# Kernel optimization log

Hardware: AMD Instinct MI355X
Metric: run time of the kernel (lower is better)

Reference implementation:

```python
import jax, jax.numpy as jnp
import numpy as np

B, T, C, H = 4, 2048, 1024, 16
D = C // H  # head_size = 64


def setup_inputs() -> dict:
    key = jax.random.key(0)
    k1, k2, k3 = jax.random.split(key, 3)
    h = jax.random.normal(k1, (B, T, C), dtype=jnp.float32)
    # additive float mask, [B,1,1,T]; zeros = no padding
    attention_mask = jnp.zeros((B, 1, 1, T), dtype=jnp.float32)
    # learned params (bias=False linears), scaled like default torch init
    w_attn = jax.random.normal(k2, (C, 3 * C), dtype=jnp.float32) / np.sqrt(C)
    w_proj = jax.random.normal(k3, (C, C), dtype=jnp.float32) / np.sqrt(C)
    return {"h": h, "attention_mask": attention_mask, "w_attn": w_attn, "w_proj": w_proj}


def reference(h, attention_mask, w_attn, w_proj):
    # fused QKV projection: [B,T,3C]
    qkv = jnp.einsum("btc,cd->btd", h, w_attn)
    q, k, v = jnp.split(qkv, 3, axis=-1)
    # [B,T,C] -> [B,H,T,D]
    def to_heads(x):
        return x.reshape(B, T, H, D).transpose(0, 2, 1, 3)
    q, k, v = to_heads(q), to_heads(k), to_heads(v)
    # scaled dot-product attention with additive mask (non-causal)
    scale = 1.0 / np.sqrt(D).astype(np.float32)
    scores = jnp.einsum("bhqd,bhkd->bhqk", q, k) * scale + attention_mask
    probs = jax.nn.softmax(scores, axis=-1)
    y = jnp.einsum("bhqk,bhkd->bhqd", probs, v)
    # [B,H,T,D] -> [B,T,C]
    y = y.transpose(0, 2, 1, 3).reshape(B, T, C)
    return jnp.einsum("btc,cd->btd", y, w_proj)
```

## Files before the change

### kernel.cpp

```cpp
#include <hip/hip_runtime.h>
#include <hip/hip_bf16.h>

#define DEV static __device__ __forceinline__

typedef __attribute__((ext_vector_type(4))) float f32x4;
typedef __attribute__((ext_vector_type(8))) short bf16x8;

constexpr int Bb = 4, Ts = 2048, Cc = 1024, Hh = 16, Dd = 64;
constexpr int Mm = Bb * Ts;
constexpr float SCQ = 0.18033688f;

union frag_u {
  bf16x8 f;
  uint2  u2[2];
  ushort us[8];
  uint4  u4;
};

DEV ushort f2bf(float x) {
  union { float f; unsigned u; } v; v.f = x;
  unsigned r = v.u + 0x7FFFu + ((v.u >> 16) & 1u);
  return (ushort)(r >> 16);
}

DEV ushort f2bf_hw(float x) {
  union { __hip_bfloat16 b; ushort u; } cv;
  cv.b = __float2bfloat16(x);
  return cv.u;
}

typedef const __attribute__((address_space(1))) unsigned int gu32;
typedef __attribute__((address_space(3))) unsigned int lu32;
DEV void gload16(const void* g, void* l) {
  __builtin_amdgcn_global_load_lds((gu32*)g, (lu32*)l, 16, 0, 0);
}

DEV void ld_frag16(frag_u& fr, const ushort* lds, int row, int chunk) {
  int off = row * 128 + ((chunk ^ (row & 7)) << 4);
  fr.u4 = *reinterpret_cast<const uint4*>(reinterpret_cast<const char*>(lds) + off);
}
DEV void lds_st64p(ushort* lds, int row, int p, uint2 v) {
  int off = row * 128 + ((((p >> 3) ^ (row & 7)) << 4) | ((2 * p) & 15));
  *reinterpret_cast<uint2*>(reinterpret_cast<char*>(lds) + off) = v;
}

__global__ __launch_bounds__(256) void cvt_kernel(const float* __restrict__ in,
                                                  ushort* __restrict__ out, int n4) {
  for (int i = blockIdx.x * blockDim.x + threadIdx.x; i < n4;
       i += gridDim.x * blockDim.x) {
    float4 v = reinterpret_cast<const float4*>(in)[i];
    ushort4 o;
    o.x = f2bf(v.x); o.y = f2bf(v.y); o.z = f2bf(v.z); o.w = f2bf(v.w);
    reinterpret_cast<ushort4*>(out)[i] = o;
  }
}

__global__ __launch_bounds__(256) void expmask_kernel(const float* __restrict__ m,
                                                      float* __restrict__ em, int n) {
  int i = blockIdx.x * blockDim.x + threadIdx.x;
  if (i < n) em[i] = __expf(m[i]);
}

__global__ __launch_bounds__(256) void transpose_cvt(const float* __restrict__ in,
                                                     ushort* __restrict__ out,
                                                     int R, int Ccols) {
  __shared__ float tile[32][33];
  int c0 = blockIdx.x * 32, r0 = blockIdx.y * 32;
  int tx = threadIdx.x & 31, ty = threadIdx.x >> 5;
#pragma unroll
  for (int i = 0; i < 4; ++i) {
    int r = ty + i * 8;
    tile[r][tx] = in[(size_t)(r0 + r) * Ccols + c0 + tx];
  }
  __syncthreads();
#pragma unroll
  for (int i = 0; i < 4; ++i) {
    int r = ty + i * 8;
    out[(size_t)(c0 + r) * R + r0 + tx] = f2bf(tile[tx][r]);
  }
}

template <int EPI>
__global__ __launch_bounds__(256) void gemm_bt(const ushort* __restrict__ A,
                                               const ushort* __restrict__ Bt,
                                               int M, int N, int K,
                                               float* __restrict__ Cf,
                                               ushort* __restrict__ Qb,
                                               ushort* __restrict__ Kb,
                                               ushort* __restrict__ Vb,
                                               const float* __restrict__ expm) {
  __shared__ ushort Al[2][128 * 64];
  __shared__ ushort Bl[2][128 * 64];
  const int tid = threadIdx.x;
  const int lane = tid & 63, wid = tid >> 6;
  const int g = lane >> 4, l15 = lane & 15;
  const int wr = wid >> 1, wc = wid & 1;
  const int m0 = blockIdx.y * 128, n0 = blockIdx.x * 128;

#define ISSUE(slot, kt)                                                         \
  {                                                                             \
    _Pragma("unroll") for (int it = 0; it < 4; ++it) {                          \
      int chunk = wid * 256 + it * 64 + lane;                                   \
      int row = chunk >> 3, c16 = (chunk & 7) ^ (row & 7);                      \
      gload16(A + (size_t)(m0 + row) * K + (kt) * 64 + c16 * 8,                 \
              Al[slot] + (size_t)(wid * 256 + it * 64) * 8);                    \
      gload16(Bt + (size_t)(n0 + row) * K + (kt) * 64 + c16 * 8,                \
              Bl[slot] + (size_t)(wid * 256 + it * 64) * 8);                    \
    }                                                                           \
  }

  f32x4 acc[4][4];
#pragma unroll
  for (int i = 0; i < 4; ++i)
#pragma unroll
    for (int j = 0; j < 4; ++j) acc[i][j] = f32x4{0.f, 0.f, 0.f, 0.f};

  const int nkt = K >> 6;
  ISSUE(0, 0);
  __syncthreads();
  for (int kt = 0; kt < nkt; ++kt) {
    const int s = kt & 1;
    if (kt + 1 < nkt) ISSUE(s ^ 1, kt + 1);
#pragma unroll
    for (int ks = 0; ks < 2; ++ks) {
      frag_u af[4], bfr[4];
#pragma unroll
      for (int i = 0; i < 4; ++i) {
        ld_frag16(af[i], Al[s], wr * 64 + i * 16 + l15, 4 * ks + g);
        ld_frag16(bfr[i], Bl[s], wc * 64 + i * 16 + l15, 4 * ks + g);
      }
#pragma unroll
      for (int i = 0; i < 4; ++i)
#pragma unroll
        for (int j = 0; j < 4; ++j)
          acc[i][j] = __builtin_amdgcn_mfma_f32_16x16x32_bf16(af[i].f, bfr[j].f,
                                                              acc[i][j], 0, 0, 0);
    }
    __syncthreads();
  }
#undef ISSUE

#pragma unroll
  for (int i = 0; i < 4; ++i)
#pragma unroll
    for (int j = 0; j < 4; ++j) {
      int mrow = m0 + wr * 64 + i * 16 + 4 * g;
      int ncol = n0 + wc * 64 + j * 16 + l15;
#pragma unroll
      for (int r = 0; r < 4; ++r) {
        float v = acc[i][j][r];
        int m = mrow + r;
        if (EPI == 0) {
          Cf[(size_t)m * N + ncol] = v;
        } else {
          int which = ncol >> 10, c = ncol & 1023;
          int hd = c >> 6, d = c & 63;
          int b = m >> 11, t = m & 2047;
          size_t idx;
          if (which == 2) {
            v *= expm[(size_t)b * Ts + t];
            idx = (((size_t)(b * Hh + hd)) * Dd + d) * Ts + t;
          } else {
            if (which == 0) v *= SCQ;
            idx = (((size_t)(b * Hh + hd)) * Ts + t) * Dd + d;
          }
          ushort bv = f2bf(v);
          ushort* dst = (which == 0) ? Qb : (which == 1) ? Kb : Vb;
          dst[idx] = bv;
        }
      }
    }
}

__global__ __launch_bounds__(512, 4) void attn_kernel(const ushort* __restrict__ Qb,
                                                      const ushort* __restrict__ Kb,
                                                      const ushort* __restrict__ VTb,
                                                      const float* __restrict__ expm,
                                                      ushort* __restrict__ Yb) {
  __shared__ ushort Klds[2][64 * 64];
  __shared__ ushort Vlds[2][64 * 64];
  __shared__ ushort wlds[2][64];

  const int tid = threadIdx.x;
  const int lane = tid & 63, wid = tid >> 6;
  const int g = lane >> 4, l15 = lane & 15;
  const int bh = blockIdx.x;
  const int b = bh >> 4, h = bh & 15;
  const int qt = blockIdx.y;

  const ushort* Qh = Qb + (size_t)bh * Ts * Dd;
  const ushort* Kh = Kb + (size_t)bh * Ts * Dd;
  const ushort* Vh = VTb + (size_t)bh * Dd * Ts;
  const float* erow = expm + (size_t)b * Ts;

  const int krow = tid >> 3, kpos = tid & 7;
  const int kc16 = kpos ^ (krow & 7);
  const int srow = tid >> 3, sc16 = tid & 7;
  const int vp0 = 32 * (sc16 >> 2) + 16 * (sc16 & 1) + 4 * ((sc16 >> 1) & 1);
  const int wp = (tid & 32) | ((tid & 12) << 1) | ((tid & 16) >> 2) | (tid & 3);

  frag_u aq[2][2];
#pragma unroll
  for (int qsub = 0; qsub < 2; ++qsub) {
    const ushort* qp = Qh + (size_t)(qt * 256 + wid * 32 + qsub * 16 + l15) * Dd;
#pragma unroll
    for (int ks = 0; ks < 2; ++ks)
      aq[qsub][ks].u4 = *reinterpret_cast<const uint4*>(qp + ks * 32 + 8 * g);
  }

  f32x4 acc[2][4];
  f32x4 lacc[2];
#pragma unroll
  for (int q = 0; q < 2; ++q) {
    lacc[q] = f32x4{0.f, 0.f, 0.f, 0.f};
#pragma unroll
    for (int dt = 0; dt < 4; ++dt) acc[q][dt] = f32x4{0.f, 0.f, 0.f, 0.f};
  }

  uint4 vreg;
  float wreg = 0.f;

#define ISSUE(kt, buf)                                                          \
  gload16(Kh + (size_t)((kt) * 64 + krow) * Dd + kc16 * 8,                      \
          Klds[buf] + (size_t)(wid * 64) * 8);                                  \
  vreg = *reinterpret_cast<const uint4*>(Vh + (size_t)srow * Ts + (kt) * 64 + sc16 * 8); \
  wreg = (tid < 64) ? erow[(kt) * 64 + tid] : 0.f;

#define COMMIT(buf)                                                             \
  lds_st64p(Vlds[buf], srow, vp0, uint2{vreg.x, vreg.y});                       \
  lds_st64p(Vlds[buf], srow, vp0 + 8, uint2{vreg.z, vreg.w});                   \
  if (tid < 64) wlds[buf][wp] = f2bf_hw(wreg);

  ISSUE(0, 0);
  COMMIT(0);
  __syncthreads();

  const int NT = Ts / 64;
  for (int kt = 0; kt < NT; ++kt) {
    const int cur = kt & 1;
    const bool more = (kt + 1 < NT);
    if (more) { ISSUE(kt + 1, cur ^ 1); }

    f32x4 s[2][4];
#pragma unroll
    for (int q = 0; q < 2; ++q)
#pragma unroll
      for (int n = 0; n < 4; ++n) s[q][n] = f32x4{0.f, 0.f, 0.f, 0.f};
    __builtin_amdgcn_s_setprio(1);
#pragma unroll
    for (int ks = 0; ks < 2; ++ks)
#pragma unroll
      for (int n = 0; n < 4; ++n) {
        frag_u bk;
        ld_frag16(bk, Klds[cur], n * 16 + l15, 4 * ks + g);
#pragma unroll
        for (int q = 0; q < 2; ++q)
          s[q][n] = __builtin_amdgcn_mfma_f32_16x16x32_bf16(bk.f, aq[q][ks].f,
                                                            s[q][n], 0, 0, 0);
      }
    __builtin_amdgcn_s_setprio(0);

    frag_u pa[2][2];
#pragma unroll
    for (int q = 0; q < 2; ++q)
#pragma unroll
      for (int n = 0; n < 4; ++n)
#pragma unroll
        for (int r = 0; r < 4; ++r)
          pa[q][n >> 1].us[(n & 1) * 4 + r] =
              f2bf_hw(__builtin_amdgcn_exp2f(s[q][n][r]));

    frag_u wf[2];
    wf[0].u4 = *reinterpret_cast<const uint4*>(&wlds[cur][8 * g]);
    wf[1].u4 = *reinterpret_cast<const uint4*>(&wlds[cur][32 + 8 * g]);
    __builtin_amdgcn_s_setprio(1);
#pragma unroll
    for (int ks = 0; ks < 2; ++ks)
#pragma unroll
      for (int q = 0; q < 2; ++q)
        lacc[q] = __builtin_amdgcn_mfma_f32_16x16x32_bf16(pa[q][ks].f, wf[ks].f,
                                                          lacc[q], 0, 0, 0);
#pragma unroll
    for (int ks = 0; ks < 2; ++ks)
#pragma unroll
      for (int dt = 0; dt < 4; ++dt) {
        frag_u bv;
        ld_frag16(bv, Vlds[cur], dt * 16 + l15, 4 * ks + g);
#pragma unroll
        for (int q = 0; q < 2; ++q)
          acc[q][dt] = __builtin_amdgcn_mfma_f32_16x16x32_bf16(pa[q][ks].f, bv.f,
                                                               acc[q][dt], 0, 0, 0);
      }
    __builtin_amdgcn_s_setprio(0);

    if (more) { COMMIT(cur ^ 1); }
    __syncthreads();
  }
#undef ISSUE
#undef COMMIT

#pragma unroll
  for (int q = 0; q < 2; ++q) {
#pragma unroll
    for (int r = 0; r < 4; ++r) {
      float inv = 1.0f / lacc[q][r];
      int t = qt * 256 + wid * 32 + q * 16 + 4 * g + r;
      size_t base = ((size_t)(b * Ts + t)) * Cc + h * Dd;
#pragma unroll
      for (int dt = 0; dt < 4; ++dt)
        Yb[base + dt * 16 + l15] = f2bf(acc[q][dt][r] * inv);
    }
  }
}

extern "C" void kernel_launch(void* const* d_in, const int* in_sizes, int n_in,
                              void* d_out, int out_size, void* d_ws, size_t ws_size,
                              hipStream_t stream) {
  const float* h    = (const float*)d_in[0];
  const float* mask = (const float*)d_in[1];
  const float* wa   = (const float*)d_in[2];
  const float* wp   = (const float*)d_in[3];
  float* out = (float*)d_out;

  char* ws = (char*)d_ws;
  ushort* hbf     = (ushort*)(ws);
  ushort* wattn_t = (ushort*)(ws + (16u << 20));
  ushort* wproj_t = (ushort*)(ws + (22u << 20));
  ushort* Qb      = (ushort*)(ws + (24u << 20));
  ushort* Kb      = (ushort*)(ws + (40u << 20));
  ushort* VTb     = (ushort*)(ws + (56u << 20));
  float*  expm    = (float*)(ws + (72u << 20));
  ushort* Ybf = hbf;

  cvt_kernel<<<2048, 256, 0, stream>>>(h, hbf, (Mm * Cc) / 4);
  expmask_kernel<<<(Bb * Ts + 255) / 256, 256, 0, stream>>>(mask, expm, Bb * Ts);
  transpose_cvt<<<dim3(3 * Cc / 32, Cc / 32), 256, 0, stream>>>(wa, wattn_t, Cc, 3 * Cc);
  transpose_cvt<<<dim3(Cc / 32, Cc / 32), 256, 0, stream>>>(wp, wproj_t, Cc, Cc);

  gemm_bt<1><<<dim3(3 * Cc / 128, Mm / 128), 256, 0, stream>>>(
      hbf, wattn_t, Mm, 3 * Cc, Cc, nullptr, Qb, Kb, VTb, expm);

  attn_kernel<<<dim3(Bb * Hh, Ts / 256), 512, 0, stream>>>(Qb, Kb, VTb, expm, Ybf);

  gemm_bt<0><<<dim3(Cc / 128, Mm / 128), 256, 0, stream>>>(
      Ybf, wproj_t, Mm, Cc, Cc, out, nullptr, nullptr, nullptr, nullptr);
}
```

Baseline: 203.4 us.

## Load GEMM B operand directly to registers and stage QKV epilogue through LDS

The GEMM no longer stages the B (weight) tile in LDS. Each wave loads its B fragments straight from global memory into double-buffered registers, and the k-loop is unrolled by two so register and LDS buffers alternate. The QKV epilogue now writes scaled bf16 results into a swizzled LDS tile and then emits coalesced 16-byte global stores for Q/K and the transposed V, replacing scattered 2-byte stores. The mask exponentials are cached once per block in shared memory. In exchange, register pressure rises and the B fragment loads from global memory are uncoalesced per-lane 16-byte reads.

```diff
diff --git a/kernel.cpp b/kernel.cpp
--- a/kernel.cpp
+++ b/kernel.cpp
@@ -42,6 +42,19 @@
 DEV void lds_st64p(ushort* lds, int row, int p, uint2 v) {
   int off = row * 128 + ((((p >> 3) ^ (row & 7)) << 4) | ((2 * p) & 15));
   *reinterpret_cast<uint2*>(reinterpret_cast<char*>(lds) + off) = v;
+}
+
+DEV void eW16(char* E, int row, int col, ushort v) {
+  int off = row * 256 + ((((col >> 3) ^ (row & 7)) << 4) | ((col & 7) * 2));
+  *reinterpret_cast<ushort*>(E + off) = v;
+}
+DEV void eW64(char* E, int row, int col, uint2 v) {
+  int off = row * 256 + ((((col >> 3) ^ (row & 7)) << 4) | ((col & 7) * 2));
+  *reinterpret_cast<uint2*>(E + off) = v;
+}
+DEV uint4 eR128(const char* E, int row, int dc) {
+  int off = row * 256 + ((dc ^ (row & 7)) << 4);
+  return *reinterpret_cast<const uint4*>(E + off);
 }
 
 __global__ __launch_bounds__(256) void cvt_kernel(const float* __restrict__ in,
@@ -90,86 +103,137 @@
                                                ushort* __restrict__ Vb,
                                                const float* __restrict__ expm) {
   __shared__ ushort Al[2][128 * 64];
-  __shared__ ushort Bl[2][128 * 64];
+  __shared__ float evals[128];
   const int tid = threadIdx.x;
   const int lane = tid & 63, wid = tid >> 6;
   const int g = lane >> 4, l15 = lane & 15;
   const int wr = wid >> 1, wc = wid & 1;
   const int m0 = blockIdx.y * 128, n0 = blockIdx.x * 128;
 
-#define ISSUE(slot, kt)                                                         \
+  if (EPI == 1 && tid < 128)
+    evals[tid] = expm[(size_t)(m0 >> 11) * Ts + (m0 & 2047) + tid];
+
+#define AISSUE(slot, t)                                                         \
   {                                                                             \
     _Pragma("unroll") for (int it = 0; it < 4; ++it) {                          \
       int chunk = wid * 256 + it * 64 + lane;                                   \
       int row = chunk >> 3, c16 = (chunk & 7) ^ (row & 7);                      \
-      gload16(A + (size_t)(m0 + row) * K + (kt) * 64 + c16 * 8,                 \
+      gload16(A + (size_t)(m0 + row) * K + (t) * 64 + c16 * 8,                  \
               Al[slot] + (size_t)(wid * 256 + it * 64) * 8);                    \
-      gload16(Bt + (size_t)(n0 + row) * K + (kt) * 64 + c16 * 8,                \
-              Bl[slot] + (size_t)(wid * 256 + it * 64) * 8);                    \
     }                                                                           \
   }
 
+#define BLOAD(breg, t)                                                          \
+  _Pragma("unroll") for (int j = 0; j < 4; ++j)                                 \
+    _Pragma("unroll") for (int ks = 0; ks < 2; ++ks)                            \
+      breg[j][ks].u4 = *reinterpret_cast<const uint4*>(                         \
+          Bt + (size_t)(n0 + wc * 64 + j * 16 + l15) * K + (t) * 64 + ks * 32 + 8 * g);
+
+#define COMPUTE(s, breg)                                                        \
+  _Pragma("unroll") for (int ks = 0; ks < 2; ++ks) {                            \
+    frag_u af[4];                                                               \
+    _Pragma("unroll") for (int i = 0; i < 4; ++i)                               \
+      ld_frag16(af[i], Al[s], wr * 64 + i * 16 + l15, 4 * ks + g);              \
+    _Pragma("unroll") for (int i = 0; i < 4; ++i)                               \
+      _Pragma("unroll") for (int j = 0; j < 4; ++j)                             \
+        acc[i][j] = __builtin_amdgcn_mfma_f32_16x16x32_bf16(af[i].f,            \
+                        breg[j][ks].f, acc[i][j], 0, 0, 0);                     \
+  }
+
   f32x4 acc[4][4];
 #pragma unroll
   for (int i = 0; i < 4; ++i)
 #pragma unroll
     for (int j = 0; j < 4; ++j) acc[i][j] = f32x4{0.f, 0.f, 0.f, 0.f};
 
+  frag_u b0[4][2], b1[4][2];
   const int nkt = K >> 6;
-  ISSUE(0, 0);
+
+  BLOAD(b0, 0);
+  AISSUE(0, 0);
   __syncthreads();
-  for (int kt = 0; kt < nkt; ++kt) {
-    const int s = kt & 1;
-    if (kt + 1 < nkt) ISSUE(s ^ 1, kt + 1);
-#pragma unroll
-    for (int ks = 0; ks < 2; ++ks) {
-      frag_u af[4], bfr[4];
+  for (int kt = 0; kt < nkt; kt += 2) {
+    BLOAD(b1, kt + 1);
+    AISSUE(1, kt + 1);
+    COMPUTE(0, b0);
+    __syncthreads();
+    if (kt + 2 < nkt) { BLOAD(b0, kt + 2); AISSUE(0, kt + 2); }
+    COMPUTE(1, b1);
+    __syncthreads();
+  }
+#undef AISSUE
+#undef BLOAD
+#undef COMPUTE
+
+  if (EPI == 0) {
+#pragma unroll
+    for (int i = 0; i < 4; ++i)
+#pragma unroll
+      for (int j = 0; j < 4; ++j) {
+        int mrow = m0 + wr * 64 + i * 16 + 4 * g;
+        int ncol = n0 + wc * 64 + j * 16 + l15;
+#pragma unroll
+        for (int r = 0; r < 4; ++r)
+          Cf[(size_t)(mrow + r) * N + ncol] = acc[i][j][r];
+      }
+  } else {
+    char* E = reinterpret_cast<char*>(&Al[0][0]);
+    const int seg = n0 >> 10;
+    const int hd0 = (n0 & 1023) >> 6;
+    const int bq = m0 >> 11, tt0 = m0 & 2047;
+    if (seg < 2) {
+      const float vs = (seg == 0) ? SCQ : 1.0f;
+#pragma unroll
+      for (int i = 0; i < 4; ++i)
+#pragma unroll
+        for (int j = 0; j < 4; ++j) {
+          int tb = wr * 64 + i * 16 + 4 * g;
+          int ncol = wc * 64 + j * 16 + l15;
+#pragma unroll
+          for (int r = 0; r < 4; ++r)
+            eW16(E, tb + r, ncol, f2bf(acc[i][j][r] * vs));
+        }
+      __syncthreads();
+      ushort* dstQ = (seg == 0) ? Qb : Kb;
+#pragma unroll
+      for (int h2 = 0; h2 < 2; ++h2) {
+        ushort* gb = dstQ + ((size_t)(bq * Hh + hd0 + h2) * Ts + tt0) * Dd;
+#pragma unroll
+        for (int k = 0; k < 4; ++k) {
+          int c = k * 256 + tid;
+          int tt = c >> 3, d16 = c & 7;
+          uint4 v = eR128(E, tt, h2 * 8 + d16);
+          *reinterpret_cast<uint4*>(gb + (size_t)c * 8) = v;
+        }
+      }
+    } else {
 #pragma unroll
       for (int i = 0; i < 4; ++i) {
-        ld_frag16(af[i], Al[s], wr * 64 + i * 16 + l15, 4 * ks + g);
-        ld_frag16(bfr[i], Bl[s], wc * 64 + i * 16 + l15, 4 * ks + g);
-      }
-#pragma unroll
-      for (int i = 0; i < 4; ++i)
-#pragma unroll
-        for (int j = 0; j < 4; ++j)
-          acc[i][j] = __builtin_amdgcn_mfma_f32_16x16x32_bf16(af[i].f, bfr[j].f,
-                                                              acc[i][j], 0, 0, 0);
+        int tb = wr * 64 + i * 16 + 4 * g;
+        float e0 = evals[tb], e1 = evals[tb + 1];
+        float e2 = evals[tb + 2], e3 = evals[tb + 3];
+#pragma unroll
+        for (int j = 0; j < 4; ++j) {
+          int ncol = wc * 64 + j * 16 + l15;
+          unsigned lo = (unsigned)f2bf(acc[i][j][0] * e0) |
+                        ((unsigned)f2bf(acc[i][j][1] * e1) << 16);
+          unsigned hi = (unsigned)f2bf(acc[i][j][2] * e2) |
+                        ((unsigned)f2bf(acc[i][j][3] * e3) << 16);
+          eW64(E, ncol, tb, uint2{lo, hi});
+        }
+      }
+      __syncthreads();
+#pragma unroll
+      for (int k = 0; k < 8; ++k) {
+        int c = k * 256 + tid;
+        int row = c >> 4, t16 = c & 15;
+        int hd = hd0 + (row >> 6), d = row & 63;
+        uint4 v = eR128(E, row, t16);
+        ushort* gb = Vb + ((size_t)(bq * Hh + hd) * Dd + d) * Ts + tt0;
+        *reinterpret_cast<uint4*>(gb + (size_t)t16 * 8) = v;
+      }
     }
-    __syncthreads();
-  }
-#undef ISSUE
-
-#pragma unroll
-  for (int i = 0; i < 4; ++i)
-#pragma unroll
-    for (int j = 0; j < 4; ++j) {
-      int mrow = m0 + wr * 64 + i * 16 + 4 * g;
-      int ncol = n0 + wc * 64 + j * 16 + l15;
-#pragma unroll
-      for (int r = 0; r < 4; ++r) {
-        float v = acc[i][j][r];
-        int m = mrow + r;
-        if (EPI == 0) {
-          Cf[(size_t)m * N + ncol] = v;
-        } else {
-          int which = ncol >> 10, c = ncol & 1023;
-          int hd = c >> 6, d = c & 63;
-          int b = m >> 11, t = m & 2047;
-          size_t idx;
-          if (which == 2) {
-            v *= expm[(size_t)b * Ts + t];
-            idx = (((size_t)(b * Hh + hd)) * Dd + d) * Ts + t;
-          } else {
-            if (which == 0) v *= SCQ;
-            idx = (((size_t)(b * Hh + hd)) * Ts + t) * Dd + d;
-          }
-          ushort bv = f2bf(v);
-          ushort* dst = (which == 0) ? Qb : (which == 1) ? Kb : Vb;
-          dst[idx] = bv;
-        }
-      }
-    }
+  }
 }
 
 __global__ __launch_bounds__(512, 4) void attn_kernel(const ushort* __restrict__ Qb,
```

Measured after the change: 251.6 us. 23.7% more time.

## Switch GEMM to 32x32 MFMA, single-buffer LDS, staged V-transpose epilogue

Applied to the files above, without the earlier changes.

The GEMM moves from 16x16x32 to 32x32x16 bf16 MFMA tiles and drops the double-buffered LDS prefetch for a single buffer with load-then-sync. This halves LDS use, which may raise occupancy, but global-to-LDS loads no longer overlap with compute. The QKV epilogue is specialised per block segment, hoisting branch decisions and caching the mask exponentials in shared memory. The transposed V output is staged through a swizzled LDS tile so it can be written with coalesced 16-byte stores instead of scattered 2-byte writes.

```diff
diff --git a/kernel.cpp b/kernel.cpp
--- a/kernel.cpp
+++ b/kernel.cpp
@@ -4,6 +4,7 @@
 #define DEV static __device__ __forceinline__
 
 typedef __attribute__((ext_vector_type(4))) float f32x4;
+typedef __attribute__((ext_vector_type(16))) float f32x16;
 typedef __attribute__((ext_vector_type(8))) short bf16x8;
 
 constexpr int Bb = 4, Ts = 2048, Cc = 1024, Hh = 16, Dd = 64;
@@ -42,6 +43,15 @@
 DEV void lds_st64p(ushort* lds, int row, int p, uint2 v) {
   int off = row * 128 + ((((p >> 3) ^ (row & 7)) << 4) | ((2 * p) & 15));
   *reinterpret_cast<uint2*>(reinterpret_cast<char*>(lds) + off) = v;
+}
+
+DEV void eW64b(char* E, int row, int col, uint2 v) {
+  int off = row * 256 + ((((col >> 3) ^ (row & 15)) << 4) | ((col & 7) * 2));
+  *reinterpret_cast<uint2*>(E + off) = v;
+}
+DEV uint4 eR128b(const char* E, int row, int dc) {
+  int off = row * 256 + ((dc ^ (row & 15)) << 4);
+  return *reinterpret_cast<const uint4*>(E + off);
 }
 
 __global__ __launch_bounds__(256) void cvt_kernel(const float* __restrict__ in,
@@ -89,87 +99,122 @@
                                                ushort* __restrict__ Kb,
                                                ushort* __restrict__ Vb,
                                                const float* __restrict__ expm) {
-  __shared__ ushort Al[2][128 * 64];
-  __shared__ ushort Bl[2][128 * 64];
+  __shared__ ushort Lds[2][128 * 64];
+  __shared__ float evals[128];
+  ushort* Al = Lds[0];
+  ushort* Bl = Lds[1];
   const int tid = threadIdx.x;
   const int lane = tid & 63, wid = tid >> 6;
-  const int g = lane >> 4, l15 = lane & 15;
+  const int l31 = lane & 31, lh = lane >> 5;
   const int wr = wid >> 1, wc = wid & 1;
   const int m0 = blockIdx.y * 128, n0 = blockIdx.x * 128;
 
-#define ISSUE(slot, kt)                                                         \
-  {                                                                             \
-    _Pragma("unroll") for (int it = 0; it < 4; ++it) {                          \
-      int chunk = wid * 256 + it * 64 + lane;                                   \
-      int row = chunk >> 3, c16 = (chunk & 7) ^ (row & 7);                      \
-      gload16(A + (size_t)(m0 + row) * K + (kt) * 64 + c16 * 8,                 \
-              Al[slot] + (size_t)(wid * 256 + it * 64) * 8);                    \
-      gload16(Bt + (size_t)(n0 + row) * K + (kt) * 64 + c16 * 8,                \
-              Bl[slot] + (size_t)(wid * 256 + it * 64) * 8);                    \
-    }                                                                           \
-  }
-
-  f32x4 acc[4][4];
-#pragma unroll
-  for (int i = 0; i < 4; ++i)
-#pragma unroll
-    for (int j = 0; j < 4; ++j) acc[i][j] = f32x4{0.f, 0.f, 0.f, 0.f};
+  if (EPI == 1 && tid < 128)
+    evals[tid] = expm[(size_t)(m0 >> 11) * Ts + (m0 & 2047) + tid];
+
+  f32x16 acc[2][2];
+#pragma unroll
+  for (int mi = 0; mi < 2; ++mi)
+#pragma unroll
+    for (int nj = 0; nj < 2; ++nj)
+#pragma unroll
+      for (int r = 0; r < 16; ++r) acc[mi][nj][r] = 0.f;
 
   const int nkt = K >> 6;
-  ISSUE(0, 0);
-  __syncthreads();
   for (int kt = 0; kt < nkt; ++kt) {
-    const int s = kt & 1;
-    if (kt + 1 < nkt) ISSUE(s ^ 1, kt + 1);
-#pragma unroll
-    for (int ks = 0; ks < 2; ++ks) {
-      frag_u af[4], bfr[4];
-#pragma unroll
-      for (int i = 0; i < 4; ++i) {
-        ld_frag16(af[i], Al[s], wr * 64 + i * 16 + l15, 4 * ks + g);
-        ld_frag16(bfr[i], Bl[s], wc * 64 + i * 16 + l15, 4 * ks + g);
-      }
-#pragma unroll
-      for (int i = 0; i < 4; ++i)
-#pragma unroll
-        for (int j = 0; j < 4; ++j)
-          acc[i][j] = __builtin_amdgcn_mfma_f32_16x16x32_bf16(af[i].f, bfr[j].f,
-                                                              acc[i][j], 0, 0, 0);
+#pragma unroll
+    for (int it = 0; it < 4; ++it) {
+      int chunk = wid * 256 + it * 64 + lane;
+      int row = chunk >> 3, c16 = (chunk & 7) ^ (row & 7);
+      gload16(A + (size_t)(m0 + row) * K + kt * 64 + c16 * 8,
+              Al + (size_t)(wid * 256 + it * 64) * 8);
+      gload16(Bt + (size_t)(n0 + row) * K + kt * 64 + c16 * 8,
+              Bl + (size_t)(wid * 256 + it * 64) * 8);
     }
     __syncthreads();
-  }
-#undef ISSUE
-
-#pragma unroll
-  for (int i = 0; i < 4; ++i)
-#pragma unroll
-    for (int j = 0; j < 4; ++j) {
-      int mrow = m0 + wr * 64 + i * 16 + 4 * g;
-      int ncol = n0 + wc * 64 + j * 16 + l15;
-#pragma unroll
-      for (int r = 0; r < 4; ++r) {
-        float v = acc[i][j][r];
-        int m = mrow + r;
-        if (EPI == 0) {
-          Cf[(size_t)m * N + ncol] = v;
-        } else {
-          int which = ncol >> 10, c = ncol & 1023;
-          int hd = c >> 6, d = c & 63;
-          int b = m >> 11, t = m & 2047;
-          size_t idx;
-          if (which == 2) {
-            v *= expm[(size_t)b * Ts + t];
-            idx = (((size_t)(b * Hh + hd)) * Dd + d) * Ts + t;
-          } else {
-            if (which == 0) v *= SCQ;
-            idx = (((size_t)(b * Hh + hd)) * Ts + t) * Dd + d;
-          }
-          ushort bv = f2bf(v);
-          ushort* dst = (which == 0) ? Qb : (which == 1) ? Kb : Vb;
-          dst[idx] = bv;
+#pragma unroll
+    for (int kk = 0; kk < 4; ++kk) {
+      const int chunk = kk * 2 + lh;
+      frag_u af[2], bfr[2];
+#pragma unroll
+      for (int mi = 0; mi < 2; ++mi)
+        ld_frag16(af[mi], Al, wr * 64 + mi * 32 + l31, chunk);
+#pragma unroll
+      for (int nj = 0; nj < 2; ++nj)
+        ld_frag16(bfr[nj], Bl, wc * 64 + nj * 32 + l31, chunk);
+#pragma unroll
+      for (int mi = 0; mi < 2; ++mi)
+#pragma unroll
+        for (int nj = 0; nj < 2; ++nj)
+          acc[mi][nj] = __builtin_amdgcn_mfma_f32_32x32x16_bf16(
+              af[mi].f, bfr[nj].f, acc[mi][nj], 0, 0, 0);
+    }
+    __syncthreads();
+  }
+
+  if (EPI == 0) {
+#pragma unroll
+    for (int mi = 0; mi < 2; ++mi)
+#pragma unroll
+      for (int nj = 0; nj < 2; ++nj) {
+        int ncol = n0 + wc * 64 + nj * 32 + l31;
+#pragma unroll
+        for (int r = 0; r < 16; ++r) {
+          int mrow = m0 + wr * 64 + mi * 32 + (r & 3) + 8 * (r >> 2) + 4 * lh;
+          Cf[(size_t)mrow * N + ncol] = acc[mi][nj][r];
         }
       }
+  } else {
+    const int seg = n0 >> 10;
+    const int hd0 = (n0 & 1023) >> 6;
+    const int bq = m0 >> 11, tt0 = m0 & 2047;
+    if (seg < 2) {
+      const float vs = (seg == 0) ? SCQ : 1.0f;
+      ushort* dstQ = (seg == 0) ? Qb : Kb;
+#pragma unroll
+      for (int mi = 0; mi < 2; ++mi)
+#pragma unroll
+        for (int nj = 0; nj < 2; ++nj) {
+          int colb = wc * 64 + nj * 32 + l31;
+          int hd = hd0 + (colb >> 6), d = colb & 63;
+          ushort* gb = dstQ + (size_t)(bq * Hh + hd) * Ts * Dd + d;
+#pragma unroll
+          for (int r = 0; r < 16; ++r) {
+            int tt = tt0 + wr * 64 + mi * 32 + (r & 3) + 8 * (r >> 2) + 4 * lh;
+            gb[(size_t)tt * Dd] = f2bf(acc[mi][nj][r] * vs);
+          }
+        }
+    } else {
+      char* E = reinterpret_cast<char*>(&Lds[0][0]);
+#pragma unroll
+      for (int mi = 0; mi < 2; ++mi)
+#pragma unroll
+        for (int nj = 0; nj < 2; ++nj) {
+          int erow = wc * 64 + nj * 32 + l31;
+#pragma unroll
+          for (int q2 = 0; q2 < 4; ++q2) {
+            int tb = wr * 64 + mi * 32 + 8 * q2 + 4 * lh;
+            float e0 = evals[tb], e1 = evals[tb + 1];
+            float e2 = evals[tb + 2], e3 = evals[tb + 3];
+            unsigned lo = (unsigned)f2bf(acc[mi][nj][4 * q2 + 0] * e0) |
+                          ((unsigned)f2bf(acc[mi][nj][4 * q2 + 1] * e1) << 16);
+            unsigned hi = (unsigned)f2bf(acc[mi][nj][4 * q2 + 2] * e2) |
+                          ((unsigned)f2bf(acc[mi][nj][4 * q2 + 3] * e3) << 16);
+            eW64b(E, erow, tb, uint2{lo, hi});
+          }
+        }
+      __syncthreads();
+#pragma unroll
+      for (int k = 0; k < 8; ++k) {
+        int c = k * 256 + tid;
+        int row = c >> 4, t16 = c & 15;
+        int hd = hd0 + (row >> 6), d = row & 63;
+        uint4 v = eR128b(E, row, t16);
+        *reinterpret_cast<uint4*>(
+            Vb + ((size_t)(bq * Hh + hd) * Dd + d) * Ts + tt0 + t16 * 8) = v;
+      }
     }
+  }
 }
 
 __global__ __launch_bounds__(512, 4) void attn_kernel(const ushort* __restrict__ Qb,
```

New measurement: 172.1 us. 15.4% less time.
